# Kernel tuning notes

Measured on AMD Instinct MI355X. Metric: run time of the kernel, lower is better.

## Reference

```python
import jax, jax.numpy as jnp
import numpy as np

B, S, M = 32, 16384, 64
IN_DIM, OUT_DIM, HID = 64, 64, 512
N_READ, N_WRITE = 1, 1
LSTM_IN = IN_DIM + OUT_DIM + M * N_READ
EPS = 1e-8  # torch F.cosine_similarity eps


def setup_inputs():
    key = jax.random.key(0)
    ks = jax.random.split(key, 16)
    w = lambda k, sh: (0.02 * jax.random.normal(k, sh)).astype(jnp.float32)
    return {
        'x_input': jax.random.normal(ks[0], (B, 1, IN_DIM), dtype=jnp.float32),
        'prev_desired_output': jax.random.normal(ks[1], (B, 1, OUT_DIM), dtype=jnp.float32),
        'prev_read_vec': jax.random.normal(ks[2], (B, 1, M * N_READ), dtype=jnp.float32),
        'memory': jax.random.normal(ks[3], (B, S, M), dtype=jnp.float32),
        'W_ih': w(ks[4], (4 * HID, LSTM_IN)),
        'W_hh': w(ks[5], (4 * HID, HID)),
        'b_ih': jnp.zeros((4 * HID,), jnp.float32),
        'b_hh': jnp.zeros((4 * HID,), jnp.float32),
        'W_r': w(ks[6], (N_READ * (M + 6), HID)),
        'b_r': jnp.zeros((N_READ * (M + 6),), jnp.float32),
        'W_w': w(ks[7], (N_WRITE * (3 * M + 6), HID)),
        'b_w': jnp.zeros((N_WRITE * (3 * M + 6),), jnp.float32),
        'W_o': w(ks[8], (OUT_DIM, HID + M * N_READ)),
        'b_o': jnp.zeros((OUT_DIM,), jnp.float32),
    }


def _addressing(h, W, b, mem, nbr_heads, is_read):
    # ctrl2head linear -> [B, H, gate_dim], then slice k/beta/g/s/gamma(/erase/add)
    out = (h @ W.T + b).reshape(h.shape[0], nbr_heads, -1)
    k = out[..., :M]
    beta = jax.nn.softplus(out[..., M:M + 1])
    g = jax.nn.sigmoid(out[..., M + 1:M + 2])
    s = jax.nn.softmax(jax.nn.softplus(out[..., M + 2:M + 5]), axis=-1)  # 3-tap shift kernel
    gamma = 1.0 + jax.nn.softplus(out[..., M + 5:M + 6])
    # content addressing: cosine similarity of key vs each slot
    dot = jnp.einsum('bhm,bsm->bhs', k, mem)
    kn = jnp.maximum(jnp.linalg.norm(k, axis=-1), EPS)   # [B,H]
    mn = jnp.maximum(jnp.linalg.norm(mem, axis=-1), EPS)  # [B,S]
    cos = dot / (kn[:, :, None] * mn[:, None, :])
    wc = jax.nn.softmax(beta * cos, axis=-1)
    # location addressing; prev_w is zeros after reset so wg = g*wc + (1-g)*0
    wg = g * wc
    # circular 3-tap shift (conv1d over circularly padded weights)
    ws = s[..., 0:1] * jnp.roll(wg, 1, axis=-1) + s[..., 1:2] * wg + s[..., 2:3] * jnp.roll(wg, -1, axis=-1)
    wgam = ws ** gamma  # sharpening
    w_final = wgam / jnp.sum(wgam, axis=-1, keepdims=True)
    if is_read:
        return w_final
    return w_final, out[..., M + 6:2 * M + 6], out[..., 2 * M + 6:3 * M + 6]


def reference(x_input, prev_desired_output, prev_read_vec, memory,
              W_ih, W_hh, b_ih, b_hh, W_r, b_r, W_w, b_w, W_o, b_o):
    # single-layer LSTM step from zero (h0, c0) = (0, 0)
    xt = jnp.concatenate([x_input, prev_desired_output, prev_read_vec], axis=2)[:, 0]
    z = xt @ W_ih.T + b_ih + b_hh  # h0 @ W_hh.T == 0
    i, f, gg, o = jnp.split(z, 4, axis=-1)
    c = jax.nn.sigmoid(i) * jnp.tanh(gg)  # c0 == 0
    h = jax.nn.sigmoid(o) * jnp.tanh(c)   # [B, HID]
    # read heads (read pre-write memory)
    w_read = _addressing(h, W_r, b_r, memory, N_READ, True)
    r = jnp.einsum('bhs,bsm->bhm', w_read, memory)  # [B, N_READ, M]
    # write heads: source per-head loop overwrites nmemory[bidx] each head,
    # so only the LAST write head takes effect -> use head -1
    w_write, erase, add = _addressing(h, W_w, b_w, memory, N_WRITE, False)
    wl, el, al = w_write[:, -1], erase[:, -1], add[:, -1]
    new_mem = memory * (1.0 - wl[:, :, None] * el[:, None, :]) + wl[:, :, None] * al[:, None, :]
    # external output: softmax(Linear(cat(h, read)))
    ext_in = jnp.concatenate([h, r.reshape(r.shape[0], -1)], axis=-1)
    output = jax.nn.softmax(ext_in @ W_o.T + b_o, axis=-1)
    return output, new_mem
```

## Files before the change

kernel.cpp:

```cpp
#include <hip/hip_runtime.h>
#include <hip/hip_bf16.h>
#include <math.h>

#define BB 32
#define SS 16384
#define MM 64
#define HID 512
#define EPSV 1e-8f

#define OFF_H    0
#define OFF_P    16384
#define OFF_SGRP 32768
#define OFF_SGWP (OFF_SGRP + BB*64)
#define OFF_RP   (OFF_SGWP + BB*64)
#define OFF_WGR  (OFF_RP + BB*64*64)
#define OFF_WGW  (OFF_WGR + BB*SS)

__device__ __forceinline__ float sigmoidf_(float x) { return 1.f / (1.f + expf(-x)); }
__device__ __forceinline__ float softplusf_(float x) {
    return (x > 0.f) ? x + log1pf(expf(-x)) : log1pf(expf(x));
}

__global__ void k_lstm(const float* __restrict__ x, const float* __restrict__ pdo,
                       const float* __restrict__ prv,
                       const float* __restrict__ W_ih, const float* __restrict__ b_ih,
                       const float* __restrict__ b_hh, float* __restrict__ ws) {
    int wid = blockIdx.x * 4 + (threadIdx.x >> 6);
    int lane = threadIdx.x & 63;
    int b = wid >> 9, t = wid & 511;
    float x0 = x[b * 64 + lane];
    float x1 = pdo[b * 64 + lane];
    float x2 = prv[b * 64 + lane];
    const float* wi = W_ih + (size_t)t * 192;
    const float* wg = W_ih + (size_t)(1024 + t) * 192;
    const float* wo = W_ih + (size_t)(1536 + t) * 192;
    float zi = x0 * wi[lane] + x1 * wi[64 + lane] + x2 * wi[128 + lane];
    float zg = x0 * wg[lane] + x1 * wg[64 + lane] + x2 * wg[128 + lane];
    float zo = x0 * wo[lane] + x1 * wo[64 + lane] + x2 * wo[128 + lane];
    #pragma unroll
    for (int off = 32; off >= 1; off >>= 1) {
        zi += __shfl_xor(zi, off);
        zg += __shfl_xor(zg, off);
        zo += __shfl_xor(zo, off);
    }
    if (lane == 0) {
        zi += b_ih[t] + b_hh[t];
        zg += b_ih[1024 + t] + b_hh[1024 + t];
        zo += b_ih[1536 + t] + b_hh[1536 + t];
        float c = sigmoidf_(zi) * tanhf(zg);
        ws[OFF_H + (size_t)b * 512 + t] = sigmoidf_(zo) * tanhf(c);
    }
}

__global__ void k_heads(const float* __restrict__ W_r, const float* __restrict__ b_r,
                        const float* __restrict__ W_w, const float* __restrict__ b_w,
                        float* __restrict__ ws) {
    int wid = blockIdx.x * 4 + (threadIdx.x >> 6);
    int lane = threadIdx.x & 63;
    int b = wid / 268, j = wid % 268;
    const float* h = ws + OFF_H + (size_t)b * 512;
    const float* wrow;
    float bias;
    if (j < 70) { wrow = W_r + (size_t)j * 512; bias = b_r[j]; }
    else        { wrow = W_w + (size_t)(j - 70) * 512; bias = b_w[j - 70]; }
    float acc = 0.f;
    #pragma unroll
    for (int c = 0; c < 8; c++) acc = fmaf(h[c * 64 + lane], wrow[c * 64 + lane], acc);
    #pragma unroll
    for (int off = 32; off >= 1; off >>= 1) acc += __shfl_xor(acc, off);
    if (lane != 0) return;
    acc += bias;
    float* P = ws + OFF_P + (size_t)b * 512;
    if (j < 70) {
        if (j < 64)       P[j] = acc;
        else if (j == 64) P[64] = softplusf_(acc);
        else if (j == 65) P[65] = sigmoidf_(acc);
        else if (j <= 68) P[96 + (j - 66)] = acc;
        else              P[69] = 1.f + softplusf_(acc);
    } else {
        int jj = j - 70;
        if (jj < 64)       P[128 + jj] = acc;
        else if (jj == 64) P[192] = softplusf_(acc);
        else if (jj == 65) P[193] = sigmoidf_(acc);
        else if (jj <= 68) P[224 + (jj - 66)] = acc;
        else if (jj == 69) P[197] = 1.f + softplusf_(acc);
        else if (jj < 134) P[256 + (jj - 70)] = acc;
        else               P[320 + (jj - 134)] = acc;
    }
}

#define PST 260
__global__ void k_scorewgam(const float* __restrict__ mem, float* __restrict__ ws) {
    int b = blockIdx.x >> 6;
    int chunk = blockIdx.x & 63;
    int tid = threadIdx.x;
    const float* P = ws + OFF_P + (size_t)b * 512;
    int row0 = chunk * 256;

    __shared__ float pdr[16 * PST], pdw[16 * PST], pn2[16 * PST];
    __shared__ float sh_er[258], sh_ew[258];
    __shared__ float par[8];
    __shared__ float lr[4], lw[4];

    if (tid < 64) {
        float kr = P[tid], kw = P[128 + tid];
        float nr = kr * kr, nw = kw * kw;
        #pragma unroll
        for (int off = 32; off >= 1; off >>= 1) {
            nr += __shfl_xor(nr, off);
            nw += __shfl_xor(nw, off);
        }
        if (tid == 0) {
            par[0] = 1.f / fmaxf(sqrtf(nr), EPSV);
            par[1] = 1.f / fmaxf(sqrtf(nw), EPSV);
            float s0 = softplusf_(P[96]), s1 = softplusf_(P[97]), s2 = softplusf_(P[98]);
            float mx = fmaxf(s0, fmaxf(s1, s2));
            float e0 = expf(s0 - mx), e1 = expf(s1 - mx), e2 = expf(s2 - mx);
            float si = 1.f / (e0 + e1 + e2);
            par[2] = e0 * si; par[3] = e1 * si; par[4] = e2 * si;
            s0 = softplusf_(P[224]); s1 = softplusf_(P[225]); s2 = softplusf_(P[226]);
            mx = fmaxf(s0, fmaxf(s1, s2));
            e0 = expf(s0 - mx); e1 = expf(s1 - mx); e2 = expf(s2 - mx);
            si = 1.f / (e0 + e1 + e2);
            par[5] = e0 * si; par[6] = e1 * si; par[7] = e2 * si;
        }
    }
    float beta_r = P[64], beta_w = P[192];
    float gamma_r = P[69], gamma_w = P[197];

    if (tid < 32) {
        int grp = tid >> 4, c = tid & 15;
        int hrow = grp ? ((row0 + 256) & (SS - 1)) : ((row0 - 1) & (SS - 1));
        float4 m4 = *(const float4*)(mem + ((size_t)b * SS + hrow) * 64 + c * 4);
        float4 kr4 = *(const float4*)(P + c * 4);
        float4 kw4 = *(const float4*)(P + 128 + c * 4);
        float dr = m4.x * kr4.x + m4.y * kr4.y + m4.z * kr4.z + m4.w * kr4.w;
        float dw = m4.x * kw4.x + m4.y * kw4.y + m4.z * kw4.z + m4.w * kw4.w;
        float n2 = m4.x * m4.x + m4.y * m4.y + m4.z * m4.z + m4.w * m4.w;
        #pragma unroll
        for (int off = 8; off >= 1; off >>= 1) {
            dr += __shfl_xor(dr, off);
            dw += __shfl_xor(dw, off);
            n2 += __shfl_xor(n2, off);
        }
        if (c == 0) {
            float imn = 1.f / fmaxf(sqrtf(n2), EPSV);
            int slot = grp ? 257 : 0;
            sh_er[slot] = exp2f(1.44269504f * beta_r * (dr * par[0] * imn - 1.f));
            sh_ew[slot] = exp2f(1.44269504f * beta_w * (dw * par[1] * imn - 1.f));
        }
    }

    int rowslot = tid >> 4, col = tid & 15;
    float4 kr4 = *(const float4*)(P + col * 4);
    float4 kw4 = *(const float4*)(P + 128 + col * 4);
    const float4* base = (const float4*)(mem + ((size_t)b * SS + row0) * 64) + tid;
    #pragma unroll
    for (int it = 0; it < 16; ++it) {
        float4 v = base[it * 256];
        int row = it * 16 + rowslot;
        pdr[col * PST + row] = v.x * kr4.x + v.y * kr4.y + v.z * kr4.z + v.w * kr4.w;
        pdw[col * PST + row] = v.x * kw4.x + v.y * kw4.y + v.z * kw4.z + v.w * kw4.w;
        pn2[col * PST + row] = v.x * v.x + v.y * v.y + v.z * v.z + v.w * v.w;
    }
    __syncthreads();

    {
        float a0, a1, a2, a3;
        a0 = pdr[0*PST+tid] + pdr[1*PST+tid];  a1 = pdr[2*PST+tid] + pdr[3*PST+tid];
        a2 = pdr[4*PST+tid] + pdr[5*PST+tid];  a3 = pdr[6*PST+tid] + pdr[7*PST+tid];
        float dr = (a0 + a1) + (a2 + a3);
        a0 = pdr[8*PST+tid] + pdr[9*PST+tid];  a1 = pdr[10*PST+tid] + pdr[11*PST+tid];
        a2 = pdr[12*PST+tid] + pdr[13*PST+tid]; a3 = pdr[14*PST+tid] + pdr[15*PST+tid];
        dr += (a0 + a1) + (a2 + a3);
        a0 = pdw[0*PST+tid] + pdw[1*PST+tid];  a1 = pdw[2*PST+tid] + pdw[3*PST+tid];
        a2 = pdw[4*PST+tid] + pdw[5*PST+tid];  a3 = pdw[6*PST+tid] + pdw[7*PST+tid];
        float dw = (a0 + a1) + (a2 + a3);
        a0 = pdw[8*PST+tid] + pdw[9*PST+tid];  a1 = pdw[10*PST+tid] + pdw[11*PST+tid];
        a2 = pdw[12*PST+tid] + pdw[13*PST+tid]; a3 = pdw[14*PST+tid] + pdw[15*PST+tid];
        dw += (a0 + a1) + (a2 + a3);
        a0 = pn2[0*PST+tid] + pn2[1*PST+tid];  a1 = pn2[2*PST+tid] + pn2[3*PST+tid];
        a2 = pn2[4*PST+tid] + pn2[5*PST+tid];  a3 = pn2[6*PST+tid] + pn2[7*PST+tid];
        float n2 = (a0 + a1) + (a2 + a3);
        a0 = pn2[8*PST+tid] + pn2[9*PST+tid];  a1 = pn2[10*PST+tid] + pn2[11*PST+tid];
        a2 = pn2[12*PST+tid] + pn2[13*PST+tid]; a3 = pn2[14*PST+tid] + pn2[15*PST+tid];
        n2 += (a0 + a1) + (a2 + a3);
        float imn = 1.f / fmaxf(sqrtf(n2), EPSV);
        sh_er[1 + tid] = exp2f(1.44269504f * beta_r * (dr * par[0] * imn - 1.f));
        sh_ew[1 + tid] = exp2f(1.44269504f * beta_w * (dw * par[1] * imn - 1.f));
    }
    __syncthreads();

    float cvr = par[2] * sh_er[tid] + par[3] * sh_er[tid + 1] + par[4] * sh_er[tid + 2];
    float cvw = par[5] * sh_ew[tid] + par[6] * sh_ew[tid + 1] + par[7] * sh_ew[tid + 2];
    float wgr = exp2f(gamma_r * log2f(cvr));
    float wgw = exp2f(gamma_w * log2f(cvw));
    ws[OFF_WGR + (size_t)b * SS + row0 + tid] = wgr;
    ws[OFF_WGW + (size_t)b * SS + row0 + tid] = wgw;

    int w = tid >> 6, lane = tid & 63;
    float rr = wgr, rw2 = wgw;
    #pragma unroll
    for (int off = 32; off >= 1; off >>= 1) {
        rr += __shfl_xor(rr, off);
        rw2 += __shfl_xor(rw2, off);
    }
    if (lane == 0) { lr[w] = rr; lw[w] = rw2; }
    __syncthreads();
    if (tid == 0) {
        ws[OFF_SGRP + b * 64 + chunk] = lr[0] + lr[1] + lr[2] + lr[3];
        ws[OFF_SGWP + b * 64 + chunk] = lw[0] + lw[1] + lw[2] + lw[3];
    }
}

__global__ void k_update(const float* __restrict__ mem, float* __restrict__ ws,
                         float* __restrict__ out) {
    int b = blockIdx.x >> 6, chunk = blockIdx.x & 63, tid = threadIdx.x;
    int rowslot = tid >> 4, col = tid & 15;
    const float* P = ws + OFF_P + (size_t)b * 512;
    float4 er4 = *(const float4*)(P + 256 + col * 4);
    float4 ad4 = *(const float4*)(P + 320 + col * 4);

    __shared__ float sinv[2];
    if (tid < 64) {
        float v = ws[OFF_SGRP + b * 64 + tid];
        #pragma unroll
        for (int off = 32; off >= 1; off >>= 1) v += __shfl_xor(v, off);
        if (tid == 0) sinv[0] = 1.f / v;
    } else if (tid < 128) {
        float v = ws[OFF_SGWP + b * 64 + (tid - 64)];
        #pragma unroll
        for (int off = 32; off >= 1; off >>= 1) v += __shfl_xor(v, off);
        if (tid == 64) sinv[1] = 1.f / v;
    }
    __syncthreads();
    float isr = sinv[0], isw = sinv[1];

    const float* wgr = ws + OFF_WGR + (size_t)b * SS;
    const float* wgw = ws + OFF_WGW + (size_t)b * SS;
    float* nm = out + 2048 + (size_t)b * SS * 64;
    float4 racc = {0.f, 0.f, 0.f, 0.f};
    int row0 = chunk * 256;
    for (int it = 0; it < 16; ++it) {
        int row = row0 + it * 16 + rowslot;
        float wr = wgr[row] * isr;
        float ww = wgw[row] * isw;
        float4 v = *(const float4*)(mem + ((size_t)b * SS + row) * 64 + col * 4);
        racc.x = fmaf(wr, v.x, racc.x);
        racc.y = fmaf(wr, v.y, racc.y);
        racc.z = fmaf(wr, v.z, racc.z);
        racc.w = fmaf(wr, v.w, racc.w);
        float4 o4;
        o4.x = v.x * (1.f - ww * er4.x) + ww * ad4.x;
        o4.y = v.y * (1.f - ww * er4.y) + ww * ad4.y;
        o4.z = v.z * (1.f - ww * er4.z) + ww * ad4.z;
        o4.w = v.w * (1.f - ww * er4.w) + ww * ad4.w;
        *(float4*)(nm + (size_t)row * 64 + col * 4) = o4;
    }
    __shared__ float4 red[256];
    red[tid] = racc;
    __syncthreads();
    if (tid < 16) {
        float4 a = red[tid];
        for (int rs = 1; rs < 16; ++rs) {
            float4 t2 = red[rs * 16 + tid];
            a.x += t2.x; a.y += t2.y; a.z += t2.z; a.w += t2.w;
        }
        float* rp = ws + OFF_RP + ((size_t)b * 64 + chunk) * 64;
        rp[tid * 4 + 0] = a.x;
        rp[tid * 4 + 1] = a.y;
        rp[tid * 4 + 2] = a.z;
        rp[tid * 4 + 3] = a.w;
    }
}

__global__ void k_out(const float* __restrict__ ws, const float* __restrict__ W_o,
                      const float* __restrict__ b_o, float* __restrict__ out) {
    int b = blockIdx.x, o = threadIdx.x;
    __shared__ float sh_r[64];
    float accr = 0.f;
    for (int c = 0; c < 64; ++c) accr += ws[OFF_RP + ((size_t)b * 64 + c) * 64 + o];
    sh_r[o] = accr;
    __syncthreads();
    const float* h = ws + OFF_H + (size_t)b * 512;
    const float* w = W_o + (size_t)o * 576;
    float acc = b_o[o];
    for (int t = 0; t < 512; t++) acc = fmaf(h[t], w[t], acc);
    for (int m = 0; m < 64; m++) acc = fmaf(sh_r[m], w[512 + m], acc);
    float mx = acc;
    #pragma unroll
    for (int off = 32; off >= 1; off >>= 1) mx = fmaxf(mx, __shfl_xor(mx, off));
    float e = expf(acc - mx);
    float sm = e;
    #pragma unroll
    for (int off = 32; off >= 1; off >>= 1) sm += __shfl_xor(sm, off);
    out[b * 64 + o] = e / sm;
}

extern "C" void kernel_launch(void* const* d_in, const int* in_sizes, int n_in,
                              void* d_out, int out_size, void* d_ws, size_t ws_size,
                              hipStream_t stream) {
    const float* x    = (const float*)d_in[0];
    const float* pdo  = (const float*)d_in[1];
    const float* prv  = (const float*)d_in[2];
    const float* mem  = (const float*)d_in[3];
    const float* W_ih = (const float*)d_in[4];
    const float* b_ih = (const float*)d_in[6];
    const float* b_hh = (const float*)d_in[7];
    const float* W_r  = (const float*)d_in[8];
    const float* b_r  = (const float*)d_in[9];
    const float* W_w  = (const float*)d_in[10];
    const float* b_w  = (const float*)d_in[11];
    const float* W_o  = (const float*)d_in[12];
    const float* b_o  = (const float*)d_in[13];
    float* out = (float*)d_out;
    float* ws  = (float*)d_ws;

    k_lstm<<<BB * 512 / 4, 256, 0, stream>>>(x, pdo, prv, W_ih, b_ih, b_hh, ws);
    k_heads<<<(BB * 268) / 4, 256, 0, stream>>>(W_r, b_r, W_w, b_w, ws);
    k_scorewgam<<<BB * 64, 256, 0, stream>>>(mem, ws);
    k_update<<<BB * 64, 256, 0, stream>>>(mem, ws, out);
    k_out<<<BB, 64, 0, stream>>>(ws, W_o, b_o, out);
}
```

Measured before the change: 99.50 us.

## Fuse scoring, memory update and output into one cooperative kernel with grid sync

Merges the score/weighting, memory update and output kernels into a single cooperative kernel of 512 blocks, each owning 1024 rows. The per-row weights stay in shared memory instead of going through global workspace, and grid.sync separates the normalisation and read-vector reduction phases. It also uses nontemporal stores for the new memory and computes dot products per row across 4 lanes. In exchange it depends on cooperative launch, which falls back to the old kernels if the launch fails, and the memory slab may be evicted from L2 between the two passes.

```diff
diff --git a/kernel.cpp b/kernel.cpp
--- a/kernel.cpp
+++ b/kernel.cpp
@@ -1,12 +1,17 @@
 #include <hip/hip_runtime.h>
+#include <hip/hip_cooperative_groups.h>
 #include <hip/hip_bf16.h>
 #include <math.h>
+
+namespace cg = cooperative_groups;
 
 #define BB 32
 #define SS 16384
 #define MM 64
 #define HID 512
 #define EPSV 1e-8f
+
+typedef float nf4 __attribute__((ext_vector_type(4)));
 
 #define OFF_H    0
 #define OFF_P    16384
@@ -15,6 +20,9 @@
 #define OFF_RP   (OFF_SGWP + BB*64)
 #define OFF_WGR  (OFF_RP + BB*64*64)
 #define OFF_WGW  (OFF_WGR + BB*SS)
+#define OFF_CSGR (OFF_WGW + BB*SS)
+#define OFF_CSGW (OFF_CSGR + BB*16)
+#define OFF_CRP  (OFF_CSGW + BB*16)
 
 __device__ __forceinline__ float sigmoidf_(float x) { return 1.f / (1.f + expf(-x)); }
 __device__ __forceinline__ float softplusf_(float x) {
@@ -89,21 +97,29 @@
     }
 }
 
-#define PST 260
-__global__ void k_scorewgam(const float* __restrict__ mem, float* __restrict__ ws) {
-    int b = blockIdx.x >> 6;
-    int chunk = blockIdx.x & 63;
+__global__ void __launch_bounds__(256, 2)
+k_main(const float* __restrict__ mem, float* __restrict__ ws,
+       const float* __restrict__ W_o, const float* __restrict__ b_o,
+       float* __restrict__ out) {
+    cg::grid_group grid = cg::this_grid();
+    int bc = blockIdx.x;
+    int b = bc >> 4, slab = bc & 15;
     int tid = threadIdx.x;
+    int r0 = slab * 1024;
     const float* P = ws + OFF_P + (size_t)b * 512;
-    int row0 = chunk * 256;
-
-    __shared__ float pdr[16 * PST], pdw[16 * PST], pn2[16 * PST];
-    __shared__ float sh_er[258], sh_ew[258];
+
+    __shared__ float sh_kr[64], sh_kw[64];
+    __shared__ float sh_er[1026], sh_ew[1026];
+    __shared__ float sh_wgr[1024], sh_wgw[1024];
     __shared__ float par[8];
     __shared__ float lr[4], lw[4];
+    __shared__ float4 red[256];
+    __shared__ float sh_r[64];
+    __shared__ float red2[256];
 
     if (tid < 64) {
         float kr = P[tid], kw = P[128 + tid];
+        sh_kr[tid] = kr; sh_kw[tid] = kw;
         float nr = kr * kr, nw = kw * kw;
         #pragma unroll
         for (int off = 32; off >= 1; off >>= 1) {
@@ -128,6 +144,208 @@
     float beta_r = P[64], beta_w = P[192];
     float gamma_r = P[69], gamma_w = P[197];
 
+    if (tid < 32) {
+        int grp = tid >> 4, c = tid & 15;
+        int hrow = grp ? ((r0 + 1024) & (SS - 1)) : ((r0 - 1) & (SS - 1));
+        float4 m4 = *(const float4*)(mem + ((size_t)b * SS + hrow) * 64 + c * 4);
+        float4 kr4 = *(const float4*)(P + c * 4);
+        float4 kw4 = *(const float4*)(P + 128 + c * 4);
+        float dr = m4.x * kr4.x + m4.y * kr4.y + m4.z * kr4.z + m4.w * kr4.w;
+        float dw = m4.x * kw4.x + m4.y * kw4.y + m4.z * kw4.z + m4.w * kw4.w;
+        float n2 = m4.x * m4.x + m4.y * m4.y + m4.z * m4.z + m4.w * m4.w;
+        #pragma unroll
+        for (int off = 8; off >= 1; off >>= 1) {
+            dr += __shfl_xor(dr, off);
+            dw += __shfl_xor(dw, off);
+            n2 += __shfl_xor(n2, off);
+        }
+        if (c == 0) {
+            float imn = 1.f / fmaxf(sqrtf(n2), EPSV);
+            int slot = grp ? 1025 : 0;
+            sh_er[slot] = exp2f(1.44269504f * beta_r * (dr * par[0] * imn - 1.f));
+            sh_ew[slot] = exp2f(1.44269504f * beta_w * (dw * par[1] * imn - 1.f));
+        }
+    }
+    __syncthreads();
+    float ikr = par[0], ikw = par[1];
+
+    int w = tid >> 6, lane = tid & 63;
+    {
+        int rw = lane >> 2, q = lane & 3;
+        float4 kr0 = *(const float4*)(sh_kr + q * 16);
+        float4 kr1 = *(const float4*)(sh_kr + q * 16 + 4);
+        float4 kr2 = *(const float4*)(sh_kr + q * 16 + 8);
+        float4 kr3 = *(const float4*)(sh_kr + q * 16 + 12);
+        float4 kw0 = *(const float4*)(sh_kw + q * 16);
+        float4 kw1 = *(const float4*)(sh_kw + q * 16 + 4);
+        float4 kw2 = *(const float4*)(sh_kw + q * 16 + 8);
+        float4 kw3 = *(const float4*)(sh_kw + q * 16 + 12);
+        #pragma unroll 2
+        for (int it = 0; it < 16; ++it) {
+            int r = w * 256 + it * 16 + rw;
+            const float4* rp = (const float4*)(mem + ((size_t)b * SS + r0 + r) * 64) + q * 4;
+            float4 a0 = rp[0], a1 = rp[1], a2 = rp[2], a3 = rp[3];
+            float dr, dw, n2;
+            dr = a0.x*kr0.x + a0.y*kr0.y + a0.z*kr0.z + a0.w*kr0.w;
+            dr = fmaf(a1.x,kr1.x, fmaf(a1.y,kr1.y, fmaf(a1.z,kr1.z, fmaf(a1.w,kr1.w, dr))));
+            dr = fmaf(a2.x,kr2.x, fmaf(a2.y,kr2.y, fmaf(a2.z,kr2.z, fmaf(a2.w,kr2.w, dr))));
+            dr = fmaf(a3.x,kr3.x, fmaf(a3.y,kr3.y, fmaf(a3.z,kr3.z, fmaf(a3.w,kr3.w, dr))));
+            dw = a0.x*kw0.x + a0.y*kw0.y + a0.z*kw0.z + a0.w*kw0.w;
+            dw = fmaf(a1.x,kw1.x, fmaf(a1.y,kw1.y, fmaf(a1.z,kw1.z, fmaf(a1.w,kw1.w, dw))));
+            dw = fmaf(a2.x,kw2.x, fmaf(a2.y,kw2.y, fmaf(a2.z,kw2.z, fmaf(a2.w,kw2.w, dw))));
+            dw = fmaf(a3.x,kw3.x, fmaf(a3.y,kw3.y, fmaf(a3.z,kw3.z, fmaf(a3.w,kw3.w, dw))));
+            n2 = a0.x*a0.x + a0.y*a0.y + a0.z*a0.z + a0.w*a0.w;
+            n2 = fmaf(a1.x,a1.x, fmaf(a1.y,a1.y, fmaf(a1.z,a1.z, fmaf(a1.w,a1.w, n2))));
+            n2 = fmaf(a2.x,a2.x, fmaf(a2.y,a2.y, fmaf(a2.z,a2.z, fmaf(a2.w,a2.w, n2))));
+            n2 = fmaf(a3.x,a3.x, fmaf(a3.y,a3.y, fmaf(a3.z,a3.z, fmaf(a3.w,a3.w, n2))));
+            dr += __shfl_xor(dr, 1); dr += __shfl_xor(dr, 2);
+            dw += __shfl_xor(dw, 1); dw += __shfl_xor(dw, 2);
+            n2 += __shfl_xor(n2, 1); n2 += __shfl_xor(n2, 2);
+            if (q == 0) {
+                float imn = 1.f / fmaxf(sqrtf(n2), EPSV);
+                sh_er[1 + r] = exp2f(1.44269504f * beta_r * (dr * ikr * imn - 1.f));
+                sh_ew[1 + r] = exp2f(1.44269504f * beta_w * (dw * ikw * imn - 1.f));
+            }
+        }
+    }
+    __syncthreads();
+
+    float sumr = 0.f, sumw = 0.f;
+    #pragma unroll
+    for (int k2 = 0; k2 < 4; ++k2) {
+        int row = tid + k2 * 256;
+        float cvr = par[2] * sh_er[row] + par[3] * sh_er[row + 1] + par[4] * sh_er[row + 2];
+        float cvw = par[5] * sh_ew[row] + par[6] * sh_ew[row + 1] + par[7] * sh_ew[row + 2];
+        float wgr = exp2f(gamma_r * log2f(cvr));
+        float wgw = exp2f(gamma_w * log2f(cvw));
+        sh_wgr[row] = wgr; sh_wgw[row] = wgw;
+        sumr += wgr; sumw += wgw;
+    }
+    #pragma unroll
+    for (int off = 32; off >= 1; off >>= 1) {
+        sumr += __shfl_xor(sumr, off);
+        sumw += __shfl_xor(sumw, off);
+    }
+    if (lane == 0) { lr[w] = sumr; lw[w] = sumw; }
+    __syncthreads();
+    if (tid == 0) {
+        ws[OFF_CSGR + b * 16 + slab] = lr[0] + lr[1] + lr[2] + lr[3];
+        ws[OFF_CSGW + b * 16 + slab] = lw[0] + lw[1] + lw[2] + lw[3];
+    }
+    grid.sync();
+
+    float sr = 0.f, sw = 0.f;
+    #pragma unroll
+    for (int c = 0; c < 16; ++c) {
+        sr += ws[OFF_CSGR + b * 16 + c];
+        sw += ws[OFF_CSGW + b * 16 + c];
+    }
+    float isr = 1.f / sr, isw = 1.f / sw;
+
+    {
+        int rowslot = tid >> 4, col = tid & 15;
+        float4 er4 = *(const float4*)(P + 256 + col * 4);
+        float4 ad4 = *(const float4*)(P + 320 + col * 4);
+        const float* mbase = mem + ((size_t)b * SS + r0) * 64;
+        float* nm = out + 2048 + ((size_t)b * SS + r0) * 64;
+        float4 racc = {0.f, 0.f, 0.f, 0.f};
+        for (int it = 0; it < 64; ++it) {
+            int row = it * 16 + rowslot;
+            float wr = sh_wgr[row] * isr;
+            float ww = sh_wgw[row] * isw;
+            float4 v = *(const float4*)(mbase + (size_t)row * 64 + col * 4);
+            racc.x = fmaf(wr, v.x, racc.x);
+            racc.y = fmaf(wr, v.y, racc.y);
+            racc.z = fmaf(wr, v.z, racc.z);
+            racc.w = fmaf(wr, v.w, racc.w);
+            nf4 o4;
+            o4.x = v.x * (1.f - ww * er4.x) + ww * ad4.x;
+            o4.y = v.y * (1.f - ww * er4.y) + ww * ad4.y;
+            o4.z = v.z * (1.f - ww * er4.z) + ww * ad4.z;
+            o4.w = v.w * (1.f - ww * er4.w) + ww * ad4.w;
+            __builtin_nontemporal_store(o4, (nf4*)(nm + (size_t)row * 64 + col * 4));
+        }
+        red[tid] = racc;
+        __syncthreads();
+        if (tid < 16) {
+            float4 a = red[tid];
+            for (int rs = 1; rs < 16; ++rs) {
+                float4 t2 = red[rs * 16 + tid];
+                a.x += t2.x; a.y += t2.y; a.z += t2.z; a.w += t2.w;
+            }
+            float* rp = ws + OFF_CRP + ((size_t)b * 16 + slab) * 64;
+            rp[tid * 4 + 0] = a.x;
+            rp[tid * 4 + 1] = a.y;
+            rp[tid * 4 + 2] = a.z;
+            rp[tid * 4 + 3] = a.w;
+        }
+    }
+    grid.sync();
+
+    if (slab == 0) {
+        int o = tid & 63, p = tid >> 6;
+        if (p == 0) {
+            float rs = 0.f;
+            for (int c = 0; c < 16; ++c) rs += ws[OFF_CRP + ((size_t)b * 16 + c) * 64 + o];
+            sh_r[o] = rs;
+        }
+        const float* h = ws + OFF_H + (size_t)b * 512;
+        const float* wv = W_o + (size_t)o * 576;
+        float acc = 0.f;
+        for (int t = p * 128; t < p * 128 + 128; ++t) acc = fmaf(h[t], wv[t], acc);
+        red2[tid] = acc;
+        __syncthreads();
+        if (p == 0) {
+            float a = red2[o] + red2[64 + o] + red2[128 + o] + red2[192 + o] + b_o[o];
+            for (int m = 0; m < 64; ++m) a = fmaf(sh_r[m], wv[512 + m], a);
+            float mx = a;
+            #pragma unroll
+            for (int off = 32; off >= 1; off >>= 1) mx = fmaxf(mx, __shfl_xor(mx, off));
+            float e = expf(a - mx);
+            float sm = e;
+            #pragma unroll
+            for (int off = 32; off >= 1; off >>= 1) sm += __shfl_xor(sm, off);
+            out[b * 64 + o] = e / sm;
+        }
+    }
+}
+
+#define PST 260
+__global__ void k_scorewgam(const float* __restrict__ mem, float* __restrict__ ws) {
+    int b = blockIdx.x >> 6;
+    int chunk = blockIdx.x & 63;
+    int tid = threadIdx.x;
+    const float* P = ws + OFF_P + (size_t)b * 512;
+    int row0 = chunk * 256;
+    __shared__ float pdr[16 * PST], pdw[16 * PST], pn2[16 * PST];
+    __shared__ float sh_er[258], sh_ew[258];
+    __shared__ float par[8];
+    __shared__ float lr[4], lw[4];
+    if (tid < 64) {
+        float kr = P[tid], kw = P[128 + tid];
+        float nr = kr * kr, nw = kw * kw;
+        #pragma unroll
+        for (int off = 32; off >= 1; off >>= 1) {
+            nr += __shfl_xor(nr, off);
+            nw += __shfl_xor(nw, off);
+        }
+        if (tid == 0) {
+            par[0] = 1.f / fmaxf(sqrtf(nr), EPSV);
+            par[1] = 1.f / fmaxf(sqrtf(nw), EPSV);
+            float s0 = softplusf_(P[96]), s1 = softplusf_(P[97]), s2 = softplusf_(P[98]);
+            float mx = fmaxf(s0, fmaxf(s1, s2));
+            float e0 = expf(s0 - mx), e1 = expf(s1 - mx), e2 = expf(s2 - mx);
+            float si = 1.f / (e0 + e1 + e2);
+            par[2] = e0 * si; par[3] = e1 * si; par[4] = e2 * si;
+            s0 = softplusf_(P[224]); s1 = softplusf_(P[225]); s2 = softplusf_(P[226]);
+            mx = fmaxf(s0, fmaxf(s1, s2));
+            e0 = expf(s0 - mx); e1 = expf(s1 - mx); e2 = expf(s2 - mx);
+            si = 1.f / (e0 + e1 + e2);
+            par[5] = e0 * si; par[6] = e1 * si; par[7] = e2 * si;
+        }
+    }
+    float beta_r = P[64], beta_w = P[192];
+    float gamma_r = P[69], gamma_w = P[197];
     if (tid < 32) {
         int grp = tid >> 4, c = tid & 15;
         int hrow = grp ? ((row0 + 256) & (SS - 1)) : ((row0 - 1) & (SS - 1));
@@ -150,7 +368,6 @@
             sh_ew[slot] = exp2f(1.44269504f * beta_w * (dw * par[1] * imn - 1.f));
         }
     }
-
     int rowslot = tid >> 4, col = tid & 15;
     float4 kr4 = *(const float4*)(P + col * 4);
     float4 kw4 = *(const float4*)(P + 128 + col * 4);
@@ -164,7 +381,6 @@
         pn2[col * PST + row] = v.x * v.x + v.y * v.y + v.z * v.z + v.w * v.w;
     }
     __syncthreads();
-
     {
         float a0, a1, a2, a3;
         a0 = pdr[0*PST+tid] + pdr[1*PST+tid];  a1 = pdr[2*PST+tid] + pdr[3*PST+tid];
@@ -190,14 +406,12 @@
         sh_ew[1 + tid] = exp2f(1.44269504f * beta_w * (dw * par[1] * imn - 1.f));
     }
     __syncthreads();
-
     float cvr = par[2] * sh_er[tid] + par[3] * sh_er[tid + 1] + par[4] * sh_er[tid + 2];
     float cvw = par[5] * sh_ew[tid] + par[6] * sh_ew[tid + 1] + par[7] * sh_ew[tid + 2];
     float wgr = exp2f(gamma_r * log2f(cvr));
     float wgw = exp2f(gamma_w * log2f(cvw));
     ws[OFF_WGR + (size_t)b * SS + row0 + tid] = wgr;
     ws[OFF_WGW + (size_t)b * SS + row0 + tid] = wgw;
-
     int w = tid >> 6, lane = tid & 63;
     float rr = wgr, rw2 = wgw;
     #pragma unroll
@@ -220,7 +434,6 @@
     const float* P = ws + OFF_P + (size_t)b * 512;
     float4 er4 = *(const float4*)(P + 256 + col * 4);
     float4 ad4 = *(const float4*)(P + 320 + col * 4);
-
     __shared__ float sinv[2];
     if (tid < 64) {
         float v = ws[OFF_SGRP + b * 64 + tid];
@@ -235,7 +448,6 @@
     }
     __syncthreads();
     float isr = sinv[0], isw = sinv[1];
-
     const float* wgr = ws + OFF_WGR + (size_t)b * SS;
     const float* wgw = ws + OFF_WGW + (size_t)b * SS;
     float* nm = out + 2048 + (size_t)b * SS * 64;
@@ -318,7 +530,15 @@
 
     k_lstm<<<BB * 512 / 4, 256, 0, stream>>>(x, pdo, prv, W_ih, b_ih, b_hh, ws);
     k_heads<<<(BB * 268) / 4, 256, 0, stream>>>(W_r, b_r, W_w, b_w, ws);
-    k_scorewgam<<<BB * 64, 256, 0, stream>>>(mem, ws);
-    k_update<<<BB * 64, 256, 0, stream>>>(mem, ws, out);
-    k_out<<<BB, 64, 0, stream>>>(ws, W_o, b_o, out);
-}
+
+    const float* memc = mem; float* wsc = ws;
+    const float* Woc = W_o; const float* boc = b_o; float* outc = out;
+    void* args[] = { (void*)&memc, (void*)&wsc, (void*)&Woc, (void*)&boc, (void*)&outc };
+    hipError_t err = hipLaunchCooperativeKernel((const void*)k_main, dim3(BB * 16),
+                                                dim3(256), args, 0, stream);
+    if (err != hipSuccess) {
+        k_scorewgam<<<BB * 64, 256, 0, stream>>>(mem, ws);
+        k_update<<<BB * 64, 256, 0, stream>>>(mem, ws, out);
+        k_out<<<BB, 64, 0, stream>>>(ws, W_o, b_o, out);
+    }
+}
```

New measurement: 223.8 us. +124.9%, slower.
